# Performance work log

Hardware: AMD Instinct MI355X
Metric: run time of the kernel (lower is better)

Reference implementation:

```python
import jax, jax.numpy as jnp
import numpy as np

D = 1024   # n_embd
H = 16     # n_head
HD = D // H

def setup_inputs() -> dict:
    key = jax.random.key(0)
    ks = jax.random.split(key, 6)
    s = 1.0 / np.sqrt(D)
    x  = jax.random.normal(ks[0], (4, 2048, D), dtype=jnp.float32)
    Wq = jax.random.uniform(ks[1], (D, D), jnp.float32, -s, s)
    Wk = jax.random.uniform(ks[2], (D, D), jnp.float32, -s, s)
    Wv = jax.random.uniform(ks[3], (D, D), jnp.float32, -s, s)
    Wp = jax.random.uniform(ks[4], (D, D), jnp.float32, -s, s)
    bp = jax.random.uniform(ks[5], (D,),   jnp.float32, -s, s)
    return {"x": x, "Wq": Wq, "Wk": Wk, "Wv": Wv, "Wp": Wp, "bp": bp}

def reference(x, Wq, Wk, Wv, Wp, bp):
    B, T, C = x.shape
    scale = 1.0 / np.sqrt(HD)
    # torch nn.Linear: y = x @ W.T
    q = (x @ Wq.T).reshape(B, T, H, HD).transpose(0, 2, 1, 3)  # [B,H,T,hd]
    k = (x @ Wk.T).reshape(B, T, H, HD).transpose(0, 2, 1, 3)
    v = (x @ Wv.T).reshape(B, T, H, HD).transpose(0, 2, 1, 3)
    att = jnp.einsum('bhqd,bhkd->bhqk', q, k) * scale           # [B,H,T,T]
    causal = jnp.tril(jnp.ones((T, T), dtype=bool))
    att = jnp.where(causal[None, None], att, -jnp.inf)
    att = jax.nn.softmax(att, axis=-1)
    y = jnp.einsum('bhqk,bhkd->bhqd', att, v)                   # [B,H,T,hd]
    y = y.transpose(0, 2, 1, 3).reshape(B, T, C)
    return y @ Wp.T + bp
```

## Files before the change

### kernel.cpp

```cpp
#include <hip/hip_runtime.h>
#include <hip/hip_bf16.h>
#include <math.h>


#define B_  4
#define T_  2048
#define D_  1024
#define H_  16
#define HD_ 64
#define M_  (B_ * T_)

typedef short bf16x8 __attribute__((ext_vector_type(8)));
typedef float f32x4  __attribute__((ext_vector_type(4)));

__device__ __forceinline__ f32x4 mfma16(bf16x8 a, bf16x8 b, f32x4 c) {
    return __builtin_amdgcn_mfma_f32_16x16x32_bf16(a, b, c, 0, 0, 0);
}

__device__ __forceinline__ void gl_lds16(const unsigned short* g, unsigned short* l) {
    __builtin_amdgcn_global_load_lds(
        (const __attribute__((address_space(1))) void*)g,
        (__attribute__((address_space(3))) void*)l, 16, 0, 0);
}

__device__ __forceinline__ unsigned short f2bf(float f) {
    union { __hip_bfloat16 h; unsigned short u; } cv;
    cv.h = __float2bfloat16(f);
    return cv.u;
}
__device__ __forceinline__ float bf2f(unsigned short u) {
    return __uint_as_float(((unsigned)u) << 16);
}
__device__ __forceinline__ float exp2_fast(float x) {
    return __builtin_amdgcn_exp2f(x);
}

struct su4 { unsigned short x, y, z, w; };

__global__ __launch_bounds__(256)
void cvt_kernel(const float* __restrict__ in, unsigned short* __restrict__ out) {
    const int i = blockIdx.x * 256 + threadIdx.x;
    const float4 v = ((const float4*)in)[i];
    su4 o;
    o.x = f2bf(v.x); o.y = f2bf(v.y); o.z = f2bf(v.z); o.w = f2bf(v.w);
    ((su4*)out)[i] = o;
}

__global__ __launch_bounds__(256)
void cvtw_kernel(const float* __restrict__ w0, const float* __restrict__ w1,
                 const float* __restrict__ w2, const float* __restrict__ w3,
                 unsigned short* __restrict__ o0, unsigned short* __restrict__ o1,
                 unsigned short* __restrict__ o2, unsigned short* __restrict__ o3) {
    const int y = blockIdx.y;
    const float* in       = (y == 0) ? w0 : (y == 1) ? w1 : (y == 2) ? w2 : w3;
    unsigned short* out   = (y == 0) ? o0 : (y == 1) ? o1 : (y == 2) ? o2 : o3;
    const int i = blockIdx.x * 256 + threadIdx.x;
    const float4 v = ((const float4*)in)[i];
    su4 o;
    o.x = f2bf(v.x); o.y = f2bf(v.y); o.z = f2bf(v.z); o.w = f2bf(v.w);
    ((su4*)out)[i] = o;
}

__global__ __launch_bounds__(256, 2)
void qkv_kernel(const unsigned short* __restrict__ X,
                const unsigned short* __restrict__ Wq,
                const unsigned short* __restrict__ Wk,
                const unsigned short* __restrict__ Wv,
                unsigned short* __restrict__ Qo,
                unsigned short* __restrict__ Ko,
                unsigned short* __restrict__ Vo)
{
    __shared__ unsigned short As[128 * 64];
    __shared__ unsigned short Bs[128 * 64];

    const int m0 = blockIdx.x * 128;
    const int by = blockIdx.y;
    const unsigned short* W = (by < 8) ? Wq : (by < 16) ? Wk : Wv;
    unsigned short*       O = (by < 8) ? Qo : (by < 16) ? Ko : Vo;
    const int n0   = (by & 7) * 128;
    const bool vsec = (by >= 16);
    const int tid  = threadIdx.x;
    const int lane = tid & 63;
    const int wv   = tid >> 6;
    const int wr   = (wv >> 1) * 64;
    const int wc   = (wv & 1) * 64;
    const int g    = lane >> 4;
    const int c    = lane & 15;

    f32x4 acc[4][4] = {};

    for (int k0 = 0; k0 < D_; k0 += 64) {
        #pragma unroll
        for (int i = 0; i < 4; ++i) {
            const int flat = i * 2048 + tid * 8;
            const int row = flat >> 6, col = flat & 63;
            gl_lds16(X + (size_t)(m0 + row) * D_ + k0 + col, As + flat);
            gl_lds16(W + (size_t)(n0 + row) * D_ + k0 + col, Bs + flat);
        }
        __syncthreads();
        #pragma unroll
        for (int kk = 0; kk < 64; kk += 32) {
            bf16x8 af[4], bg[4];
            #pragma unroll
            for (int mi = 0; mi < 4; ++mi)
                af[mi] = *(const bf16x8*)(As + (wr + mi * 16 + c) * 64 + kk + g * 8);
            #pragma unroll
            for (int ni = 0; ni < 4; ++ni)
                bg[ni] = *(const bf16x8*)(Bs + (wc + ni * 16 + c) * 64 + kk + g * 8);
            if (!vsec) {
                #pragma unroll
                for (int mi = 0; mi < 4; ++mi)
                    #pragma unroll
                    for (int ni = 0; ni < 4; ++ni)
                        acc[mi][ni] = mfma16(af[mi], bg[ni], acc[mi][ni]);
            } else {
                #pragma unroll
                for (int mi = 0; mi < 4; ++mi)
                    #pragma unroll
                    for (int ni = 0; ni < 4; ++ni)
                        acc[mi][ni] = mfma16(bg[ni], af[mi], acc[mi][ni]);
            }
        }
        __syncthreads();
    }

    if (!vsec) {
        #pragma unroll
        for (int mi = 0; mi < 4; ++mi)
            #pragma unroll
            for (int ni = 0; ni < 4; ++ni)
                #pragma unroll
                for (int r = 0; r < 4; ++r) {
                    const int m = m0 + wr + mi * 16 + g * 4 + r;
                    const int n = n0 + wc + ni * 16 + c;
                    const int b = m >> 11, t = m & (T_ - 1);
                    const int h = n >> 6,  hd = n & 63;
                    O[((size_t)((b << 4) + h) * T_ + t) * HD_ + hd] = f2bf(acc[mi][ni][r]);
                }
    } else {
        #pragma unroll
        for (int mi = 0; mi < 4; ++mi)
            #pragma unroll
            for (int ni = 0; ni < 4; ++ni)
                #pragma unroll
                for (int r = 0; r < 4; ++r) {
                    const int n = n0 + wc + ni * 16 + g * 4 + r;
                    const int m = m0 + wr + mi * 16 + c;
                    const int b = m >> 11, t = m & (T_ - 1);
                    const int h = n >> 6,  hd = n & 63;
                    O[((size_t)((b << 4) + h) * HD_ + hd) * T_ + t] = f2bf(acc[mi][ni][r]);
                }
    }
}

__device__ __forceinline__ bf16x8 ptrans(const f32x4& p0, const f32x4& p1,
                                         int lane, int g, int c) {
    unsigned int P32[2][2];
    P32[0][0] = (unsigned int)f2bf(p0[0]) | ((unsigned int)f2bf(p0[1]) << 16);
    P32[0][1] = (unsigned int)f2bf(p0[2]) | ((unsigned int)f2bf(p0[3]) << 16);
    P32[1][0] = (unsigned int)f2bf(p1[0]) | ((unsigned int)f2bf(p1[1]) << 16);
    P32[1][1] = (unsigned int)f2bf(p1[2]) | ((unsigned int)f2bf(p1[3]) << 16);
    const int sl0 = c + ((lane & 16) << 1);
    const int sl1 = sl0 + 16;
    const int q00 = __shfl((int)P32[0][0], sl0), q10 = __shfl((int)P32[1][0], sl0);
    const int q01 = __shfl((int)P32[0][1], sl0), q11 = __shfl((int)P32[1][1], sl0);
    const int q02 = __shfl((int)P32[0][0], sl1), q12 = __shfl((int)P32[1][0], sl1);
    const int q03 = __shfl((int)P32[0][1], sl1), q13 = __shfl((int)P32[1][1], sl1);
    const bool nhi = (g & 2) != 0;
    union { unsigned int u[4]; bf16x8 v; } pf;
    pf.u[0] = nhi ? q10 : q00;
    pf.u[1] = nhi ? q11 : q01;
    pf.u[2] = nhi ? q12 : q02;
    pf.u[3] = nhi ? q13 : q03;
    return pf.v;
}

__global__ __launch_bounds__(256, 4)
void attn_kernel(const unsigned short* __restrict__ Q,
                 const unsigned short* __restrict__ K,
                 const unsigned short* __restrict__ VT,
                 unsigned short* __restrict__ Y)
{
    __shared__ unsigned short Ks[2][4096];
    __shared__ unsigned short Vs[2][4096];

    const int bh = blockIdx.x;
    const int qt = 31 - blockIdx.y;
    const unsigned short* Qp  = Q  + (size_t)bh * T_ * HD_;
    const unsigned short* Kp  = K  + (size_t)bh * T_ * HD_;
    const unsigned short* VTp = VT + (size_t)bh * HD_ * T_;
    const int b = bh >> 4, h = bh & 15;

    const int tid  = threadIdx.x;
    const int lane = tid & 63;
    const int w    = tid >> 6;
    const int g    = lane >> 4;
    const int c    = lane & 15;
    const float SC = 0.18033688011112042f;

    const int qw = qt * 64 + w * 16;
    const int nt = qt + 1;

    int srow[2], scol[2];
    #pragma unroll
    for (int i = 0; i < 2; ++i) {
        const int L = (i * 256 + tid) * 16;
        srow[i] = L >> 7;
        scol[i] = (L & 127) ^ ((srow[i] & 7) << 4);
    }

    bf16x8 qf[2];
    #pragma unroll
    for (int dk = 0; dk < 2; ++dk) {
        bf16x8 t = *(const bf16x8*)(Qp + (size_t)(qw + c) * HD_ + dk * 32 + g * 8);
        #pragma unroll
        for (int j = 0; j < 8; ++j)
            t[j] = (short)f2bf(bf2f((unsigned short)t[j]) * SC);
        qf[dk] = t;
    }

    float m_l = -1e30f, l_l = 0.f;
    f32x4 oacc[4] = {};
    const int swz = (c & 7) << 4;

    auto stage = [&](int buf, int tb) {
        #pragma unroll
        for (int i = 0; i < 2; ++i) {
            const int L = (i * 256 + tid) * 16;
            gl_lds16(Kp + (size_t)(tb + srow[i]) * HD_ + (scol[i] >> 1),
                     &Ks[buf][L >> 1]);
            gl_lds16(VTp + (size_t)srow[i] * T_ + tb + (scol[i] >> 1),
                     &Vs[buf][L >> 1]);
        }
    };

    auto compute = [&](const unsigned short* Kbuf, const unsigned short* Vbuf,
                       int tb, bool last) {
        const char* Kb = (const char*)Kbuf;
        const char* Vb = (const char*)Vbuf;

        __builtin_amdgcn_s_setprio(1);

        f32x4 sA[2] = {}, sB[2] = {};
        #pragma unroll
        for (int ni = 0; ni < 2; ++ni)
            #pragma unroll
            for (int dk = 0; dk < 2; ++dk) {
                const int col = (dk * 64 + g * 16) ^ swz;
                const bf16x8 kA = *(const bf16x8*)(Kb + (ni * 16 + c) * 128 + col);
                const bf16x8 kB = *(const bf16x8*)(Kb + (32 + ni * 16 + c) * 128 + col);
                sA[ni] = mfma16(kA, qf[dk], sA[ni]);
                sB[ni] = mfma16(kB, qf[dk], sB[ni]);
            }

        if (last) {
            #pragma unroll
            for (int ni = 0; ni < 2; ++ni)
                #pragma unroll
                for (int r = 0; r < 4; ++r) {
                    const int kA = tb + ni * 16 + g * 4 + r;
                    sA[ni][r] = (kA      <= qw + c) ? sA[ni][r] : -1e30f;
                    sB[ni][r] = (kA + 32 <= qw + c) ? sB[ni][r] : -1e30f;
                }
        }

        float pmax = sA[0][0];
        #pragma unroll
        for (int ni = 0; ni < 2; ++ni)
            #pragma unroll
            for (int r = 0; r < 4; ++r) {
                pmax = fmaxf(pmax, sA[ni][r]);
                pmax = fmaxf(pmax, sB[ni][r]);
            }
        pmax = fmaxf(pmax, __shfl_xor(pmax, 16));
        pmax = fmaxf(pmax, __shfl_xor(pmax, 32));

        const bool skip = __all(pmax - m_l <= 8.0f);
        float al = 1.f;
        if (!skip) {
            const float mn = fmaxf(m_l, pmax);
            al = exp2_fast(m_l - mn);
            m_l = mn;
        }

        float rs = 0.f;
        #pragma unroll
        for (int ni = 0; ni < 2; ++ni)
            #pragma unroll
            for (int r = 0; r < 4; ++r) {
                const float eA = exp2_fast(sA[ni][r] - m_l);
                const float eB = exp2_fast(sB[ni][r] - m_l);
                sA[ni][r] = eA; sB[ni][r] = eB;
                rs += eA + eB;
            }
        rs += __shfl_xor(rs, 16);
        rs += __shfl_xor(rs, 32);
        l_l = l_l * al + rs;

        const bf16x8 pfA = ptrans(sA[0], sA[1], lane, g, c);
        const bf16x8 pfB = ptrans(sB[0], sB[1], lane, g, c);

        #pragma unroll
        for (int dn = 0; dn < 4; ++dn) {
            const int row = dn * 16 + c;
            const bf16x8 vA = *(const bf16x8*)(Vb + row * 128 + ((g * 16)      ^ swz));
            const bf16x8 vB = *(const bf16x8*)(Vb + row * 128 + ((64 + g * 16) ^ swz));
            if (!skip) {
                #pragma unroll
                for (int r = 0; r < 4; ++r)
                    oacc[dn][r] *= al;
            }
            oacc[dn] = mfma16(vA, pfA, oacc[dn]);
            oacc[dn] = mfma16(vB, pfB, oacc[dn]);
        }

        __builtin_amdgcn_s_setprio(0);
    };

    stage(0, 0);
    __syncthreads();
    int ti = 0;
    for (;;) {
        if (ti + 1 < nt) stage(1, (ti + 1) << 6);
        compute(Ks[0], Vs[0], ti << 6, ti == nt - 1);
        __syncthreads();
        if (++ti >= nt) break;

        if (ti + 1 < nt) stage(0, (ti + 1) << 6);
        compute(Ks[1], Vs[1], ti << 6, ti == nt - 1);
        __syncthreads();
        if (++ti >= nt) break;
    }

    const float li = 1.f / l_l;
    const size_t rowoff = (size_t)(b * T_ + qw + c) * D_ + h * 64;
    #pragma unroll
    for (int dn = 0; dn < 4; ++dn) {
        const unsigned int u0 = (unsigned int)f2bf(oacc[dn][0] * li)
                              | ((unsigned int)f2bf(oacc[dn][1] * li) << 16);
        const unsigned int u1 = (unsigned int)f2bf(oacc[dn][2] * li)
                              | ((unsigned int)f2bf(oacc[dn][3] * li) << 16);
        uint2 st; st.x = u0; st.y = u1;
        *(uint2*)(Y + rowoff + dn * 16 + g * 4) = st;
    }
}

__global__ __launch_bounds__(256, 2)
void proj_kernel(const unsigned short* __restrict__ Yin,
                 const unsigned short* __restrict__ Wp,
                 const float* __restrict__ bp,
                 float* __restrict__ Out)
{
    __shared__ unsigned short As[128 * 64];
    __shared__ unsigned short Bs[128 * 64];

    const int m0 = blockIdx.x * 128;
    const int n0 = blockIdx.y * 128;
    const int tid  = threadIdx.x;
    const int lane = tid & 63;
    const int wv   = tid >> 6;
    const int wr   = (wv >> 1) * 64;
    const int wc   = (wv & 1) * 64;
    const int g    = lane >> 4;
    const int c    = lane & 15;

    f32x4 acc[4][4] = {};

    for (int k0 = 0; k0 < D_; k0 += 64) {
        #pragma unroll
        for (int i = 0; i < 4; ++i) {
            const int flat = i * 2048 + tid * 8;
            const int row = flat >> 6, col = flat & 63;
            gl_lds16(Yin + (size_t)(m0 + row) * D_ + k0 + col, As + flat);
            gl_lds16(Wp  + (size_t)(n0 + row) * D_ + k0 + col, Bs + flat);
        }
        __syncthreads();
        #pragma unroll
        for (int kk = 0; kk < 64; kk += 32) {
            bf16x8 af[4], bg[4];
            #pragma unroll
            for (int mi = 0; mi < 4; ++mi)
                af[mi] = *(const bf16x8*)(As + (wr + mi * 16 + c) * 64 + kk + g * 8);
            #pragma unroll
            for (int ni = 0; ni < 4; ++ni)
                bg[ni] = *(const bf16x8*)(Bs + (wc + ni * 16 + c) * 64 + kk + g * 8);
            #pragma unroll
            for (int mi = 0; mi < 4; ++mi)
                #pragma unroll
                for (int ni = 0; ni < 4; ++ni)
                    acc[mi][ni] = mfma16(af[mi], bg[ni], acc[mi][ni]);
        }
        __syncthreads();
    }

    #pragma unroll
    for (int mi = 0; mi < 4; ++mi) {
        #pragma unroll
        for (int ni = 0; ni < 4; ++ni) {
            const int n = n0 + wc + ni * 16 + c;
            const float bb = bp[n];
            #pragma unroll
            for (int r = 0; r < 4; ++r) {
                const int m = m0 + wr + mi * 16 + g * 4 + r;
                Out[(size_t)m * D_ + n] = acc[mi][ni][r] + bb;
            }
        }
    }
}

extern "C" void kernel_launch(void* const* d_in, const int* in_sizes, int n_in,
                              void* d_out, int out_size, void* d_ws, size_t ws_size,
                              hipStream_t stream) {
    const float* x  = (const float*)d_in[0];
    const float* Wq = (const float*)d_in[1];
    const float* Wk = (const float*)d_in[2];
    const float* Wv = (const float*)d_in[3];
    const float* Wp = (const float*)d_in[4];
    const float* bp = (const float*)d_in[5];
    float* out = (float*)d_out;

    const size_t SZ  = (size_t)M_ * D_;
    const size_t WSZ = (size_t)D_ * D_;
    unsigned short* ws = (unsigned short*)d_ws;
    unsigned short* XB  = ws;
    unsigned short* WQB = XB  + SZ;
    unsigned short* WKB = WQB + WSZ;
    unsigned short* WVB = WKB + WSZ;
    unsigned short* WPB = WVB + WSZ;
    unsigned short* Qw  = WPB + WSZ;
    unsigned short* Kw  = Qw + SZ;
    unsigned short* Vw  = Kw + SZ;
    unsigned short* Yw  = XB;

    dim3 blk(256);
    cvt_kernel <<<dim3(SZ / 1024),     blk, 0, stream>>>(x, XB);
    cvtw_kernel<<<dim3(WSZ / 1024, 4), blk, 0, stream>>>(Wq, Wk, Wv, Wp, WQB, WKB, WVB, WPB);

    qkv_kernel <<<dim3(M_ / 128, 24), blk, 0, stream>>>(XB, WQB, WKB, WVB, Qw, Kw, Vw);
    attn_kernel<<<dim3(B_ * H_, T_ / 64), blk, 0, stream>>>(Qw, Kw, Vw, Yw);
    proj_kernel<<<dim3(M_ / 128, D_ / 128), blk, 0, stream>>>(Yw, WPB, bp, out);
}
```

Before: 196.0 us.

## Process 128 query rows per attention block with two 16-row strips per wave

Each attention workgroup now covers 128 query rows instead of 64: every wave holds two 16-row Q strips with separate softmax state and accumulators. Each K/V tile staged in LDS is reused across twice as many query rows, and K fragments are loaded into registers once and shared by both strips. Strips that lie entirely above the causal diagonal are skipped per tile. The cost is higher register pressure, which may reduce occupancy under launch_bounds(256,4), and a grid half the size with more causal imbalance between blocks.

Measured after the change: 210.6 us. 1.07x slower.

```diff
diff --git a/kernel.cpp b/kernel.cpp
--- a/kernel.cpp
+++ b/kernel.cpp
@@ -185,7 +185,7 @@
     __shared__ unsigned short Vs[2][4096];
 
     const int bh = blockIdx.x;
-    const int qt = 31 - blockIdx.y;
+    const int qt = 15 - blockIdx.y;
     const unsigned short* Qp  = Q  + (size_t)bh * T_ * HD_;
     const unsigned short* Kp  = K  + (size_t)bh * T_ * HD_;
     const unsigned short* VTp = VT + (size_t)bh * HD_ * T_;
@@ -198,8 +198,9 @@
     const int c    = lane & 15;
     const float SC = 0.18033688011112042f;
 
-    const int qw = qt * 64 + w * 16;
-    const int nt = qt + 1;
+    const int qw0 = qt * 128 + w * 32;
+    const int qw1 = qw0 + 16;
+    const int nt  = 2 * qt + 2;
 
     int srow[2], scol[2];
     #pragma unroll
@@ -209,18 +210,22 @@
         scol[i] = (L & 127) ^ ((srow[i] & 7) << 4);
     }
 
-    bf16x8 qf[2];
+    bf16x8 qf0[2], qf1[2];
     #pragma unroll
     for (int dk = 0; dk < 2; ++dk) {
-        bf16x8 t = *(const bf16x8*)(Qp + (size_t)(qw + c) * HD_ + dk * 32 + g * 8);
-        #pragma unroll
-        for (int j = 0; j < 8; ++j)
-            t[j] = (short)f2bf(bf2f((unsigned short)t[j]) * SC);
-        qf[dk] = t;
-    }
-
-    float m_l = -1e30f, l_l = 0.f;
-    f32x4 oacc[4] = {};
+        bf16x8 t0 = *(const bf16x8*)(Qp + (size_t)(qw0 + c) * HD_ + dk * 32 + g * 8);
+        bf16x8 t1 = *(const bf16x8*)(Qp + (size_t)(qw1 + c) * HD_ + dk * 32 + g * 8);
+        #pragma unroll
+        for (int j = 0; j < 8; ++j) {
+            t0[j] = (short)f2bf(bf2f((unsigned short)t0[j]) * SC);
+            t1[j] = (short)f2bf(bf2f((unsigned short)t1[j]) * SC);
+        }
+        qf0[dk] = t0;
+        qf1[dk] = t1;
+    }
+
+    float m0 = -1e30f, l0 = 0.f, m1 = -1e30f, l1 = 0.f;
+    f32x4 oacc0[4] = {}, oacc1[4] = {};
     const int swz = (c & 7) << 4;
 
     auto stage = [&](int buf, int tb) {
@@ -234,36 +239,18 @@
         }
     };
 
-    auto compute = [&](const unsigned short* Kbuf, const unsigned short* Vbuf,
-                       int tb, bool last) {
-        const char* Kb = (const char*)Kbuf;
-        const char* Vb = (const char*)Vbuf;
-
-        __builtin_amdgcn_s_setprio(1);
-
-        f32x4 sA[2] = {}, sB[2] = {};
-        #pragma unroll
-        for (int ni = 0; ni < 2; ++ni)
-            #pragma unroll
-            for (int dk = 0; dk < 2; ++dk) {
-                const int col = (dk * 64 + g * 16) ^ swz;
-                const bf16x8 kA = *(const bf16x8*)(Kb + (ni * 16 + c) * 128 + col);
-                const bf16x8 kB = *(const bf16x8*)(Kb + (32 + ni * 16 + c) * 128 + col);
-                sA[ni] = mfma16(kA, qf[dk], sA[ni]);
-                sB[ni] = mfma16(kB, qf[dk], sB[ni]);
-            }
-
-        if (last) {
+    auto strip_sm = [&](f32x4 (&sA)[2], f32x4 (&sB)[2], int tb, int qws, bool domask,
+                        float& m_l, float& l_l, bf16x8& pfA, bf16x8& pfB, bool& skip) {
+        if (domask) {
             #pragma unroll
             for (int ni = 0; ni < 2; ++ni)
                 #pragma unroll
                 for (int r = 0; r < 4; ++r) {
                     const int kA = tb + ni * 16 + g * 4 + r;
-                    sA[ni][r] = (kA      <= qw + c) ? sA[ni][r] : -1e30f;
-                    sB[ni][r] = (kA + 32 <= qw + c) ? sB[ni][r] : -1e30f;
+                    sA[ni][r] = (kA      <= qws + c) ? sA[ni][r] : -1e30f;
+                    sB[ni][r] = (kA + 32 <= qws + c) ? sB[ni][r] : -1e30f;
                 }
         }
-
         float pmax = sA[0][0];
         #pragma unroll
         for (int ni = 0; ni < 2; ++ni)
@@ -275,14 +262,13 @@
         pmax = fmaxf(pmax, __shfl_xor(pmax, 16));
         pmax = fmaxf(pmax, __shfl_xor(pmax, 32));
 
-        const bool skip = __all(pmax - m_l <= 8.0f);
+        skip = __all(pmax - m_l <= 8.0f);
         float al = 1.f;
         if (!skip) {
             const float mn = fmaxf(m_l, pmax);
             al = exp2_fast(m_l - mn);
             m_l = mn;
         }
-
         float rs = 0.f;
         #pragma unroll
         for (int ni = 0; ni < 2; ++ni)
@@ -296,22 +282,77 @@
         rs += __shfl_xor(rs, 16);
         rs += __shfl_xor(rs, 32);
         l_l = l_l * al + rs;
-
-        const bf16x8 pfA = ptrans(sA[0], sA[1], lane, g, c);
-        const bf16x8 pfB = ptrans(sB[0], sB[1], lane, g, c);
+        pfA = ptrans(sA[0], sA[1], lane, g, c);
+        pfB = ptrans(sB[0], sB[1], lane, g, c);
+        return al;
+    };
+
+    auto compute = [&](const unsigned short* Kbuf, const unsigned short* Vbuf, int tb) {
+        const char* Kb = (const char*)Kbuf;
+        const char* Vb = (const char*)Vbuf;
+        const bool act0 = (qw0 + 15 >= tb);
+        const bool act1 = (qw1 + 15 >= tb);
+        if (!act1) return;
+
+        __builtin_amdgcn_s_setprio(1);
+
+        bf16x8 kf[8];
+        #pragma unroll
+        for (int s = 0; s < 2; ++s)
+            #pragma unroll
+            for (int ni = 0; ni < 2; ++ni)
+                #pragma unroll
+                for (int dk = 0; dk < 2; ++dk)
+                    kf[s * 4 + ni * 2 + dk] = *(const bf16x8*)(Kb
+                        + (s * 32 + ni * 16 + c) * 128 + ((dk * 64 + g * 16) ^ swz));
+
+        f32x4 s0A[2] = {}, s0B[2] = {}, s1A[2] = {}, s1B[2] = {};
+        if (act0) {
+            #pragma unroll
+            for (int ni = 0; ni < 2; ++ni)
+                #pragma unroll
+                for (int dk = 0; dk < 2; ++dk) {
+                    s0A[ni] = mfma16(kf[ni * 2 + dk],     qf0[dk], s0A[ni]);
+                    s0B[ni] = mfma16(kf[4 + ni * 2 + dk], qf0[dk], s0B[ni]);
+                }
+        }
+        #pragma unroll
+        for (int ni = 0; ni < 2; ++ni)
+            #pragma unroll
+            for (int dk = 0; dk < 2; ++dk) {
+                s1A[ni] = mfma16(kf[ni * 2 + dk],     qf1[dk], s1A[ni]);
+                s1B[ni] = mfma16(kf[4 + ni * 2 + dk], qf1[dk], s1B[ni]);
+            }
+
+        const bool dm0 = (tb + 63 > qw0);
+        const bool dm1 = (tb + 63 > qw1);
+        bf16x8 pf0A, pf0B, pf1A, pf1B;
+        bool sk0 = true, sk1 = true;
+        float al0 = 1.f, al1 = 1.f;
+        if (act0) al0 = strip_sm(s0A, s0B, tb, qw0, dm0, m0, l0, pf0A, pf0B, sk0);
+        al1 = strip_sm(s1A, s1B, tb, qw1, dm1, m1, l1, pf1A, pf1B, sk1);
 
         #pragma unroll
         for (int dn = 0; dn < 4; ++dn) {
             const int row = dn * 16 + c;
             const bf16x8 vA = *(const bf16x8*)(Vb + row * 128 + ((g * 16)      ^ swz));
             const bf16x8 vB = *(const bf16x8*)(Vb + row * 128 + ((64 + g * 16) ^ swz));
-            if (!skip) {
+            if (act0) {
+                if (!sk0) {
+                    #pragma unroll
+                    for (int r = 0; r < 4; ++r)
+                        oacc0[dn][r] *= al0;
+                }
+                oacc0[dn] = mfma16(vA, pf0A, oacc0[dn]);
+                oacc0[dn] = mfma16(vB, pf0B, oacc0[dn]);
+            }
+            if (!sk1) {
                 #pragma unroll
                 for (int r = 0; r < 4; ++r)
-                    oacc[dn][r] *= al;
-            }
-            oacc[dn] = mfma16(vA, pfA, oacc[dn]);
-            oacc[dn] = mfma16(vB, pfB, oacc[dn]);
+                    oacc1[dn][r] *= al1;
+            }
+            oacc1[dn] = mfma16(vA, pf1A, oacc1[dn]);
+            oacc1[dn] = mfma16(vB, pf1B, oacc1[dn]);
         }
 
         __builtin_amdgcn_s_setprio(0);
@@ -319,29 +360,32 @@
 
     stage(0, 0);
     __syncthreads();
-    int ti = 0;
-    for (;;) {
-        if (ti + 1 < nt) stage(1, (ti + 1) << 6);
-        compute(Ks[0], Vs[0], ti << 6, ti == nt - 1);
-        __syncthreads();
-        if (++ti >= nt) break;
-
-        if (ti + 1 < nt) stage(0, (ti + 1) << 6);
-        compute(Ks[1], Vs[1], ti << 6, ti == nt - 1);
-        __syncthreads();
-        if (++ti >= nt) break;
-    }
-
-    const float li = 1.f / l_l;
-    const size_t rowoff = (size_t)(b * T_ + qw + c) * D_ + h * 64;
+    for (int ti = 0; ti < nt; ti += 2) {
+        stage(1, (ti + 1) << 6);
+        compute(Ks[0], Vs[0], ti << 6);
+        __syncthreads();
+        if (ti + 2 < nt) stage(0, (ti + 2) << 6);
+        compute(Ks[1], Vs[1], (ti + 1) << 6);
+        __syncthreads();
+    }
+
+    const float li0 = 1.f / l0;
+    const float li1 = 1.f / l1;
+    const size_t ro0 = (size_t)(b * T_ + qw0 + c) * D_ + h * 64;
+    const size_t ro1 = (size_t)(b * T_ + qw1 + c) * D_ + h * 64;
     #pragma unroll
     for (int dn = 0; dn < 4; ++dn) {
-        const unsigned int u0 = (unsigned int)f2bf(oacc[dn][0] * li)
-                              | ((unsigned int)f2bf(oacc[dn][1] * li) << 16);
-        const unsigned int u1 = (unsigned int)f2bf(oacc[dn][2] * li)
-                              | ((unsigned int)f2bf(oacc[dn][3] * li) << 16);
-        uint2 st; st.x = u0; st.y = u1;
-        *(uint2*)(Y + rowoff + dn * 16 + g * 4) = st;
+        uint2 st0, st1;
+        st0.x = (unsigned int)f2bf(oacc0[dn][0] * li0)
+              | ((unsigned int)f2bf(oacc0[dn][1] * li0) << 16);
+        st0.y = (unsigned int)f2bf(oacc0[dn][2] * li0)
+              | ((unsigned int)f2bf(oacc0[dn][3] * li0) << 16);
+        st1.x = (unsigned int)f2bf(oacc1[dn][0] * li1)
+              | ((unsigned int)f2bf(oacc1[dn][1] * li1) << 16);
+        st1.y = (unsigned int)f2bf(oacc1[dn][2] * li1)
+              | ((unsigned int)f2bf(oacc1[dn][3] * li1) << 16);
+        *(uint2*)(Y + ro0 + dn * 16 + g * 4) = st0;
+        *(uint2*)(Y + ro1 + dn * 16 + g * 4) = st1;
     }
 }
 
@@ -437,6 +481,6 @@
     cvtw_kernel<<<dim3(WSZ / 1024, 4), blk, 0, stream>>>(Wq, Wk, Wv, Wp, WQB, WKB, WVB, WPB);
 
     qkv_kernel <<<dim3(M_ / 128, 24), blk, 0, stream>>>(XB, WQB, WKB, WVB, Qw, Kw, Vw);
-    attn_kernel<<<dim3(B_ * H_, T_ / 64), blk, 0, stream>>>(Qw, Kw, Vw, Yw);
+    attn_kernel<<<dim3(B_ * H_, 16), blk, 0, stream>>>(Qw, Kw, Vw, Yw);
     proj_kernel<<<dim3(M_ / 128, D_ / 128), blk, 0, stream>>>(Yw, WPB, bp, out);
 }
```

## Enlarge attention blocks to 128 query rows with 512 threads and merge conversion kernels

Applied to the files above, without the earlier changes.

The attention kernel now handles 128 query rows per block using 8 waves and 512 threads. Each K/V tile loaded into LDS is therefore shared by twice as many query rows, and the grid shrinks to 16 query tiles per head, launched in a reordered sequence meant to balance the causal workload. Warps whose rows are entirely above the diagonal skip the tile, and causal masking applies per warp instead of only on the final tile. The two fp32-to-bf16 conversion kernels become one kernel that writes into the workspace contiguously, saving a launch. Risks include idle waves on the skipped diagonal tiles and pressure from the larger block at 8-wave occupancy.

Result: slower. 207.4 us (+5.8%).

```diff
diff --git a/kernel.cpp b/kernel.cpp
--- a/kernel.cpp
+++ b/kernel.cpp
@@ -38,27 +38,25 @@
 struct su4 { unsigned short x, y, z, w; };
 
 __global__ __launch_bounds__(256)
-void cvt_kernel(const float* __restrict__ in, unsigned short* __restrict__ out) {
+void cvt_all_kernel(const float* __restrict__ x,
+                    const float* __restrict__ Wq, const float* __restrict__ Wk,
+                    const float* __restrict__ Wv, const float* __restrict__ Wp,
+                    unsigned short* __restrict__ dst) {
     const int i = blockIdx.x * 256 + threadIdx.x;
-    const float4 v = ((const float4*)in)[i];
+    const float* src;
+    int j;
+    if (i < 2097152) {
+        src = x; j = i;
+    } else {
+        const int k = i - 2097152;
+        const int wsel = k >> 18;
+        j = k & 262143;
+        src = (wsel == 0) ? Wq : (wsel == 1) ? Wk : (wsel == 2) ? Wv : Wp;
+    }
+    const float4 v = ((const float4*)src)[j];
     su4 o;
     o.x = f2bf(v.x); o.y = f2bf(v.y); o.z = f2bf(v.z); o.w = f2bf(v.w);
-    ((su4*)out)[i] = o;
-}
-
-__global__ __launch_bounds__(256)
-void cvtw_kernel(const float* __restrict__ w0, const float* __restrict__ w1,
-                 const float* __restrict__ w2, const float* __restrict__ w3,
-                 unsigned short* __restrict__ o0, unsigned short* __restrict__ o1,
-                 unsigned short* __restrict__ o2, unsigned short* __restrict__ o3) {
-    const int y = blockIdx.y;
-    const float* in       = (y == 0) ? w0 : (y == 1) ? w1 : (y == 2) ? w2 : w3;
-    unsigned short* out   = (y == 0) ? o0 : (y == 1) ? o1 : (y == 2) ? o2 : o3;
-    const int i = blockIdx.x * 256 + threadIdx.x;
-    const float4 v = ((const float4*)in)[i];
-    su4 o;
-    o.x = f2bf(v.x); o.y = f2bf(v.y); o.z = f2bf(v.z); o.w = f2bf(v.w);
-    ((su4*)out)[i] = o;
+    ((su4*)dst)[i] = o;
 }
 
 __global__ __launch_bounds__(256, 2)
@@ -175,7 +173,7 @@
     return pf.v;
 }
 
-__global__ __launch_bounds__(256, 4)
+__global__ __launch_bounds__(512, 8)
 void attn_kernel(const unsigned short* __restrict__ Q,
                  const unsigned short* __restrict__ K,
                  const unsigned short* __restrict__ VT,
@@ -185,7 +183,8 @@
     __shared__ unsigned short Vs[2][4096];
 
     const int bh = blockIdx.x;
-    const int qt = 31 - blockIdx.y;
+    const int by = blockIdx.y;
+    const int qt = (by < 8) ? (15 - by) : (by < 12) ? (by - 4) : (by - 12);
     const unsigned short* Qp  = Q  + (size_t)bh * T_ * HD_;
     const unsigned short* Kp  = K  + (size_t)bh * T_ * HD_;
     const unsigned short* VTp = VT + (size_t)bh * HD_ * T_;
@@ -198,16 +197,12 @@
     const int c    = lane & 15;
     const float SC = 0.18033688011112042f;
 
-    const int qw = qt * 64 + w * 16;
-    const int nt = qt + 1;
-
-    int srow[2], scol[2];
-    #pragma unroll
-    for (int i = 0; i < 2; ++i) {
-        const int L = (i * 256 + tid) * 16;
-        srow[i] = L >> 7;
-        scol[i] = (L & 127) ^ ((srow[i] & 7) << 4);
-    }
+    const int qw = qt * 128 + w * 16;
+    const int nt = 2 * qt + 2;
+
+    const int L    = tid * 16;
+    const int srow = L >> 7;
+    const int scol = (L & 127) ^ ((srow & 7) << 4);
 
     bf16x8 qf[2];
     #pragma unroll
@@ -224,20 +219,15 @@
     const int swz = (c & 7) << 4;
 
     auto stage = [&](int buf, int tb) {
-        #pragma unroll
-        for (int i = 0; i < 2; ++i) {
-            const int L = (i * 256 + tid) * 16;
-            gl_lds16(Kp + (size_t)(tb + srow[i]) * HD_ + (scol[i] >> 1),
-                     &Ks[buf][L >> 1]);
-            gl_lds16(VTp + (size_t)srow[i] * T_ + tb + (scol[i] >> 1),
-                     &Vs[buf][L >> 1]);
-        }
+        gl_lds16(Kp + (size_t)(tb + srow) * HD_ + (scol >> 1), &Ks[buf][L >> 1]);
+        gl_lds16(VTp + (size_t)srow * T_ + tb + (scol >> 1),   &Vs[buf][L >> 1]);
     };
 
-    auto compute = [&](const unsigned short* Kbuf, const unsigned short* Vbuf,
-                       int tb, bool last) {
+    auto compute = [&](const unsigned short* Kbuf, const unsigned short* Vbuf, int tb) {
+        if (tb > qw + 15) return;
         const char* Kb = (const char*)Kbuf;
         const char* Vb = (const char*)Vbuf;
+        const bool dm = (tb + 63 > qw);
 
         __builtin_amdgcn_s_setprio(1);
 
@@ -253,7 +243,7 @@
                 sB[ni] = mfma16(kB, qf[dk], sB[ni]);
             }
 
-        if (last) {
+        if (dm) {
             #pragma unroll
             for (int ni = 0; ni < 2; ++ni)
                 #pragma unroll
@@ -319,17 +309,13 @@
 
     stage(0, 0);
     __syncthreads();
-    int ti = 0;
-    for (;;) {
-        if (ti + 1 < nt) stage(1, (ti + 1) << 6);
-        compute(Ks[0], Vs[0], ti << 6, ti == nt - 1);
-        __syncthreads();
-        if (++ti >= nt) break;
-
-        if (ti + 1 < nt) stage(0, (ti + 1) << 6);
-        compute(Ks[1], Vs[1], ti << 6, ti == nt - 1);
-        __syncthreads();
-        if (++ti >= nt) break;
+    for (int ti = 0; ti < nt; ti += 2) {
+        stage(1, (ti + 1) << 6);
+        compute(Ks[0], Vs[0], ti << 6);
+        __syncthreads();
+        if (ti + 2 < nt) stage(0, (ti + 2) << 6);
+        compute(Ks[1], Vs[1], (ti + 1) << 6);
+        __syncthreads();
     }
 
     const float li = 1.f / l_l;
@@ -433,10 +419,9 @@
     unsigned short* Yw  = XB;
 
     dim3 blk(256);
-    cvt_kernel <<<dim3(SZ / 1024),     blk, 0, stream>>>(x, XB);
-    cvtw_kernel<<<dim3(WSZ / 1024, 4), blk, 0, stream>>>(Wq, Wk, Wv, Wp, WQB, WKB, WVB, WPB);
+    cvt_all_kernel<<<dim3(12288), blk, 0, stream>>>(x, Wq, Wk, Wv, Wp, ws);
 
     qkv_kernel <<<dim3(M_ / 128, 24), blk, 0, stream>>>(XB, WQB, WKB, WVB, Qw, Kw, Vw);
-    attn_kernel<<<dim3(B_ * H_, T_ / 64), blk, 0, stream>>>(Qw, Kw, Vw, Yw);
+    attn_kernel<<<dim3(B_ * H_, 16), dim3(512), 0, stream>>>(Qw, Kw, Vw, Yw);
     proj_kernel<<<dim3(M_ / 128, D_ / 128), blk, 0, stream>>>(Yw, WPB, bp, out);
 }
```
